# Kernel optimization log

Hardware: AMD Instinct MI355X
Metric: run time of the kernel (lower is better)

The kernel has to match this reference:

```python
import jax, jax.numpy as jnp
import numpy as np

B, N, D, U = 8, 2048, 512, 128


def setup_inputs() -> dict:
    key = jax.random.key(0)
    k_x, k_q, k_k, k_v, k_o = jax.random.split(key, 5)
    scale_in = 1.0 / np.sqrt(D)
    scale_u = 1.0 / np.sqrt(U)
    return {
        "inputs": jax.random.normal(k_x, (B, N, D), dtype=jnp.float32),
        "W_q": jax.random.normal(k_q, (D, U), dtype=jnp.float32) * scale_in,
        "W_k": jax.random.normal(k_k, (D, U), dtype=jnp.float32) * scale_in,
        "W_v": jax.random.normal(k_v, (D, U), dtype=jnp.float32) * scale_in,
        "W_o": jax.random.normal(k_o, (U, D), dtype=jnp.float32) * scale_u,
        "b_o": jnp.zeros((D,), dtype=jnp.float32),
    }


def reference(inputs, W_q, W_k, W_v, W_o, b_o):
    # Single-head scaled dot-product self-attention + output dense + residual
    Q = jnp.einsum('bnd,du->bnu', inputs, W_q)
    K = jnp.einsum('bnd,du->bnu', inputs, W_k)
    V = jnp.einsum('bnd,du->bnu', inputs, W_v)
    inv_sqrt_u = 1.0 / jnp.sqrt(jnp.asarray(W_q.shape[-1], inputs.dtype))
    scores = jnp.einsum('bnu,bmu->bnm', Q, K) * inv_sqrt_u  # [B,N,N]
    attn = jax.nn.softmax(scores, axis=-1)
    ctx = jnp.einsum('bnm,bmu->bnu', attn, V)  # [B,N,U]
    return jnp.einsum('bnu,ud->bnd', ctx, W_o) + b_o + inputs
```

## Files before the change

### kernel.cpp

```cpp
#include <hip/hip_runtime.h>

#define BB 8
#define NN 2048
#define DD 512
#define UU 128
#define SPLITS 4
#define KSPLIT 512

typedef __bf16 bf16_t;
typedef __bf16 bf16x4 __attribute__((ext_vector_type(4)));
typedef __bf16 bf16x8 __attribute__((ext_vector_type(8)));
typedef float floatx4 __attribute__((ext_vector_type(4)));

__device__ __forceinline__ floatx4 mfma16(bf16x8 a, bf16x8 b, floatx4 c) {
  return __builtin_amdgcn_mfma_f32_16x16x32_bf16(a, b, c, 0, 0, 0);
}

#define SW(r, g) ((((g) ^ ((r) & 7)) * 8))

__device__ __forceinline__ void gld_lds16(const bf16_t* g, bf16_t* l) {
  __builtin_amdgcn_global_load_lds(
      (const __attribute__((address_space(1))) unsigned int*)g,
      (__attribute__((address_space(3))) unsigned int*)l, 16, 0, 0);
}

__global__ __launch_bounds__(256) void cast_x_kernel(const float* __restrict__ x,
                                                     bf16_t* __restrict__ xb) {
  int G = blockIdx.x * 256 + threadIdx.x;
  int token = G >> 6;
  int g = G & 63;
  int dstg = (g & 56) | ((g & 7) ^ (token & 7));
  const float4* src = reinterpret_cast<const float4*>(x) + (size_t)G * 2;
  float4 a = src[0], b = src[1];
  bf16x8 o;
  o[0] = (bf16_t)a.x; o[1] = (bf16_t)a.y; o[2] = (bf16_t)a.z; o[3] = (bf16_t)a.w;
  o[4] = (bf16_t)b.x; o[5] = (bf16_t)b.y; o[6] = (bf16_t)b.z; o[7] = (bf16_t)b.w;
  *reinterpret_cast<bf16x8*>(&xb[(size_t)token * 512 + dstg * 8]) = o;
}

__global__ __launch_bounds__(256) void pack_w_kernel(const float* __restrict__ wq,
                                                     const float* __restrict__ wk,
                                                     const float* __restrict__ wv,
                                                     const float* __restrict__ wo,
                                                     bf16_t* __restrict__ wqkvt,
                                                     bf16_t* __restrict__ wot) {
  int gid = blockIdx.x * 256 + threadIdx.x;
  if (gid < 384 * 512) {
    int nrow = gid >> 9;
    int kdst = gid & 511;
    int ksrc = (kdst & ~56) | (((((kdst >> 3) & 7)) ^ (nrow & 7)) << 3);
    const float* src = (nrow < 128) ? wq : ((nrow < 256) ? wk : wv);
    int n = nrow & 127;
    wqkvt[gid] = (bf16_t)src[ksrc * 128 + n];
  } else {
    int g = gid - 384 * 512;
    int nrow = g >> 7;
    int kdst = g & 127;
    int ksrc = (kdst & ~56) | (((((kdst >> 3) & 7)) ^ (nrow & 7)) << 3);
    wot[g] = (bf16_t)wo[ksrc * 512 + nrow];
  }
}

__global__ __launch_bounds__(256, 4) void qkv_gemm_kernel(const bf16_t* __restrict__ xb,
                                                          const bf16_t* __restrict__ wqkvt,
                                                          bf16_t* __restrict__ Q,
                                                          bf16_t* __restrict__ K,
                                                          bf16_t* __restrict__ Vt) {
  __shared__ bf16_t lA[128 * 64];
  __shared__ bf16_t lB[64 * 64];
  const int lid = (blockIdx.x & 7) * 96 + (blockIdx.x >> 3);
  const int m0 = (lid / 6) * 128;
  const int n0 = (lid % 6) * 64;
  const int tid = threadIdx.x;
  const int w = tid >> 6, lane = tid & 63;
  const int quad = lane >> 4, l15 = lane & 15;

  floatx4 zero4 = {0.f, 0.f, 0.f, 0.f};
  floatx4 acc[2][4];
#pragma unroll
  for (int mi = 0; mi < 2; mi++)
#pragma unroll
    for (int nt = 0; nt < 4; nt++) acc[mi][nt] = zero4;

  for (int kc = 0; kc < 512; kc += 64) {
    __syncthreads();
#pragma unroll
    for (int i = 0; i < 4; i++) {
      int t = tid + i * 256;
      int r = t >> 3, g = t & 7;
      gld_lds16(&xb[(size_t)(m0 + r) * 512 + kc + g * 8], &lA[t * 8]);
    }
#pragma unroll
    for (int i = 0; i < 2; i++) {
      int t = tid + i * 256;
      int r = t >> 3, g = t & 7;
      gld_lds16(&wqkvt[(size_t)(n0 + r) * 512 + kc + g * 8], &lB[t * 8]);
    }
    asm volatile("s_waitcnt vmcnt(0)" ::: "memory");
    __syncthreads();
#pragma unroll
    for (int kb = 0; kb < 2; kb++) {
      bf16x8 bfr[4];
#pragma unroll
      for (int nt = 0; nt < 4; nt++)
        bfr[nt] = *reinterpret_cast<const bf16x8*>(
            &lB[(nt * 16 + l15) * 64 + SW(l15, kb * 4 + quad)]);
#pragma unroll
      for (int mi = 0; mi < 2; mi++) {
        bf16x8 a = *reinterpret_cast<const bf16x8*>(
            &lA[(w * 32 + mi * 16 + l15) * 64 + SW(l15, kb * 4 + quad)]);
#pragma unroll
        for (int nt = 0; nt < 4; nt++)
          acc[mi][nt] = mfma16(a, bfr[nt], acc[mi][nt]);
      }
    }
  }

#pragma unroll
  for (int mi = 0; mi < 2; mi++)
#pragma unroll
    for (int nt = 0; nt < 4; nt++) {
      int n = n0 + nt * 16 + l15;
#pragma unroll
      for (int r = 0; r < 4; r++) {
        int token = m0 + w * 32 + mi * 16 + quad * 4 + r;
        bf16_t h = (bf16_t)acc[mi][nt][r];
        if (n < 128) {
          Q[(size_t)token * 128 + n] = h;
        } else if (n < 256) {
          int nk = n - 128;
          int nsw = (nk & ~56) | ((((nk >> 3) & 7) ^ (token & 7)) << 3);
          K[(size_t)token * 128 + nsw] = h;
        } else {
          int bidx = token >> 11;
          int t = token & 2047;
          int u = n - 256;
          int tsw = (t & ~56) | ((((t >> 3) & 7) ^ (u & 7)) << 3);
          Vt[((size_t)bidx * 128 + u) * 2048 + tsw] = h;
        }
      }
    }
}

__global__ __launch_bounds__(256, 2) void attn_kernel(const bf16_t* __restrict__ Q,
                                                      const bf16_t* __restrict__ K,
                                                      const bf16_t* __restrict__ Vt,
                                                      bf16_t* __restrict__ Op,
                                                      float* __restrict__ ml) {
  __shared__ bf16_t lK[2][64 * 128];
  __shared__ bf16_t lV[2][128 * 64];
  __shared__ bf16_t lP[4][32 * 64];

  const int lid = (blockIdx.x & 7) * 64 + (blockIdx.x >> 3);
  const int qb = lid & 15;
  const int bs = lid >> 4;
  const int b = bs >> 2;
  const int s = bs & 3;
  const int tid = threadIdx.x;
  const int w = tid >> 6, lane = tid & 63;
  const int quad = lane >> 4, l15 = lane & 15;
  const float c = 0.08838834764831845f * 1.4426950408889634f;

  bf16x8 qf[2][4];
#pragma unroll
  for (int mt = 0; mt < 2; mt++) {
    const bf16_t* qrow =
        &Q[((size_t)b * NN + qb * 128 + w * 32 + mt * 16 + l15) * 128 + quad * 8];
#pragma unroll
    for (int kb = 0; kb < 4; kb++)
      qf[mt][kb] = *reinterpret_cast<const bf16x8*>(qrow + kb * 32);
  }

  float l_part[2] = {0.f, 0.f};
  floatx4 zero4 = {0.f, 0.f, 0.f, 0.f};
  floatx4 accO[2][8];
#pragma unroll
  for (int mt = 0; mt < 2; mt++)
#pragma unroll
    for (int ut = 0; ut < 8; ut++) accO[mt][ut] = zero4;

  bf16_t* pw = &lP[w][0];
  const int kt0 = s * KSPLIT;
  const bf16_t* kbase = &K[(size_t)b * NN * 128];
  const bf16_t* vbase = &Vt[(size_t)b * 128 * 2048];

  {
    const bf16_t* ksrc = kbase + (size_t)kt0 * 128;
#pragma unroll
    for (int i = 0; i < 4; i++) {
      int t = tid + i * 256;
      gld_lds16(ksrc + (size_t)t * 8, &lK[0][t * 8]);
    }
#pragma unroll
    for (int i = 0; i < 4; i++) {
      int t = tid + i * 256;
      int r = t >> 3, g = t & 7;
      gld_lds16(vbase + (size_t)r * 2048 + kt0 + g * 8, &lV[0][t * 8]);
    }
  }
  asm volatile("s_waitcnt vmcnt(0)" ::: "memory");
  __syncthreads();

  int cur = 0;
  for (int kt = kt0; kt < kt0 + KSPLIT; kt += 64) {
    if (kt + 64 < kt0 + KSPLIT) {
      const int nxt = kt + 64;
      const bf16_t* ksrc = kbase + (size_t)nxt * 128;
#pragma unroll
      for (int i = 0; i < 4; i++) {
        int t = tid + i * 256;
        gld_lds16(ksrc + (size_t)t * 8, &lK[cur ^ 1][t * 8]);
      }
#pragma unroll
      for (int i = 0; i < 4; i++) {
        int t = tid + i * 256;
        int r = t >> 3, g = t & 7;
        gld_lds16(vbase + (size_t)r * 2048 + nxt + g * 8, &lV[cur ^ 1][t * 8]);
      }
    }

    floatx4 accS[4][2];
#pragma unroll
    for (int km = 0; km < 4; km++)
#pragma unroll
      for (int mt = 0; mt < 2; mt++) accS[km][mt] = zero4;
    __builtin_amdgcn_s_setprio(1);
#pragma unroll
    for (int kb = 0; kb < 4; kb++) {
#pragma unroll
      for (int km = 0; km < 4; km++) {
        bf16x8 kf = *reinterpret_cast<const bf16x8*>(
            &lK[cur][(km * 16 + l15) * 128 + SW(l15, kb * 4 + quad)]);
#pragma unroll
        for (int mt = 0; mt < 2; mt++)
          accS[km][mt] = mfma16(kf, qf[mt][kb], accS[km][mt]);
      }
    }
    __builtin_amdgcn_s_setprio(0);

#pragma unroll
    for (int km = 0; km < 4; km++) {
#pragma unroll
      for (int mt = 0; mt < 2; mt++) {
        float p0 = __builtin_amdgcn_exp2f(accS[km][mt][0] * c);
        float p1 = __builtin_amdgcn_exp2f(accS[km][mt][1] * c);
        float p2 = __builtin_amdgcn_exp2f(accS[km][mt][2] * c);
        float p3 = __builtin_amdgcn_exp2f(accS[km][mt][3] * c);
        l_part[mt] += (p0 + p1) + (p2 + p3);
        bf16x4 pk;
        pk[0] = (bf16_t)p0; pk[1] = (bf16_t)p1; pk[2] = (bf16_t)p2; pk[3] = (bf16_t)p3;
        int row = mt * 16 + l15;
        int g = km * 2 + (quad >> 1);
        *reinterpret_cast<bf16x4*>(
            &pw[row * 64 + ((g ^ (row & 7)) * 8) + (quad & 1) * 4]) = pk;
      }
    }
    asm volatile("s_waitcnt lgkmcnt(0)" ::: "memory");

    __builtin_amdgcn_s_setprio(1);
#pragma unroll
    for (int kb = 0; kb < 2; kb++) {
      bf16x8 pa[2];
#pragma unroll
      for (int mt = 0; mt < 2; mt++)
        pa[mt] = *reinterpret_cast<const bf16x8*>(
            &pw[(mt * 16 + l15) * 64 + SW(l15, kb * 4 + quad)]);
#pragma unroll
      for (int ut = 0; ut < 8; ut++) {
        bf16x8 bv = *reinterpret_cast<const bf16x8*>(
            &lV[cur][(ut * 16 + l15) * 64 + SW(l15, kb * 4 + quad)]);
#pragma unroll
        for (int mt = 0; mt < 2; mt++)
          accO[mt][ut] = mfma16(pa[mt], bv, accO[mt][ut]);
      }
    }
    __builtin_amdgcn_s_setprio(0);

    asm volatile("s_waitcnt vmcnt(0)" ::: "memory");
    __syncthreads();
    cur ^= 1;
  }

#pragma unroll
  for (int mt = 0; mt < 2; mt++) {
    float v = l_part[mt];
    v += __shfl_xor(v, 16);
    v += __shfl_xor(v, 32);
    l_part[mt] = v;
  }

  size_t base = ((size_t)(b * 16 + qb) * SPLITS + s);
  bf16_t* op = Op + base * (128 * 128);
  float* mlp = ml + base * 128;
#pragma unroll
  for (int mt = 0; mt < 2; mt++)
#pragma unroll
    for (int ut = 0; ut < 8; ut++)
#pragma unroll
      for (int r = 0; r < 4; r++)
        op[(w * 32 + mt * 16 + quad * 4 + r) * 128 + ut * 16 + l15] =
            (bf16_t)accO[mt][ut][r];
  if (quad == 0) {
#pragma unroll
    for (int mt = 0; mt < 2; mt++) mlp[w * 32 + mt * 16 + l15] = l_part[mt];
  }
}

__global__ __launch_bounds__(256) void merge_kernel(const bf16_t* __restrict__ Op,
                                                    const float* __restrict__ ml,
                                                    bf16_t* __restrict__ ctx) {
  const int blk = blockIdx.x;
  const int qloc = blockIdx.y * 16 + (threadIdx.x >> 4);
  const int g = threadIdx.x & 15;

  float L = 0.f;
  float o[8];
#pragma unroll
  for (int j = 0; j < 8; j++) o[j] = 0.f;
#pragma unroll
  for (int s = 0; s < SPLITS; s++) {
    size_t e = (size_t)blk * SPLITS + s;
    L += ml[e * 128 + qloc];
    bf16x8 ch = *reinterpret_cast<const bf16x8*>(&Op[(e * 128 + qloc) * 128 + g * 8]);
#pragma unroll
    for (int j = 0; j < 8; j++) o[j] += (float)ch[j];
  }
  float inv = 1.0f / L;
  int gsw = (g & 8) | ((g & 7) ^ (qloc & 7));
  bf16x8 ch;
#pragma unroll
  for (int j = 0; j < 8; j++) ch[j] = (bf16_t)(o[j] * inv);
  const int bb = blk >> 4, qbl = blk & 15;
  *reinterpret_cast<bf16x8*>(
      &ctx[((size_t)bb * NN + qbl * 128 + qloc) * 128 + gsw * 8]) = ch;
}

__global__ __launch_bounds__(256, 4) void out_gemm_kernel(const bf16_t* __restrict__ ctx,
                                                          const bf16_t* __restrict__ wot,
                                                          const float* __restrict__ bo,
                                                          const float* __restrict__ x0,
                                                          float* __restrict__ out) {
  __shared__ bf16_t lA[64 * 128];
  __shared__ bf16_t lB[64 * 128];
  const int lid = (blockIdx.x & 7) * 256 + (blockIdx.x >> 3);
  const int m0 = (lid >> 3) * 64;
  const int n0 = (lid & 7) * 64;
  const int tid = threadIdx.x;
  const int w = tid >> 6, lane = tid & 63;
  const int quad = lane >> 4, l15 = lane & 15;

#pragma unroll
  for (int i = 0; i < 4; i++) {
    int t = tid + i * 256;
    gld_lds16(&ctx[(size_t)m0 * 128 + t * 8], &lA[t * 8]);
    gld_lds16(&wot[(size_t)n0 * 128 + t * 8], &lB[t * 8]);
  }
  asm volatile("s_waitcnt vmcnt(0)" ::: "memory");
  __syncthreads();

  floatx4 zero4 = {0.f, 0.f, 0.f, 0.f};
  floatx4 acc[4];
#pragma unroll
  for (int nt = 0; nt < 4; nt++) acc[nt] = zero4;
#pragma unroll
  for (int kb = 0; kb < 4; kb++) {
    bf16x8 a = *reinterpret_cast<const bf16x8*>(&lA[(w * 16 + l15) * 128 + SW(l15, kb * 4 + quad)]);
#pragma unroll
    for (int nt = 0; nt < 4; nt++) {
      bf16x8 bfr = *reinterpret_cast<const bf16x8*>(&lB[(nt * 16 + l15) * 128 + SW(l15, kb * 4 + quad)]);
      acc[nt] = mfma16(a, bfr, acc[nt]);
    }
  }

#pragma unroll
  for (int nt = 0; nt < 4; nt++) {
    int n = n0 + nt * 16 + l15;
    float bias = bo[n];
#pragma unroll
    for (int r = 0; r < 4; r++) {
      size_t m = m0 + w * 16 + quad * 4 + r;
      out[m * 512 + n] = acc[nt][r] + bias + x0[m * 512 + n];
    }
  }
}

extern "C" void kernel_launch(void* const* d_in, const int* in_sizes, int n_in,
                              void* d_out, int out_size, void* d_ws, size_t ws_size,
                              hipStream_t stream) {
  const float* x  = (const float*)d_in[0];
  const float* wq = (const float*)d_in[1];
  const float* wk = (const float*)d_in[2];
  const float* wv = (const float*)d_in[3];
  const float* wo = (const float*)d_in[4];
  const float* bo = (const float*)d_in[5];
  float* out = (float*)d_out;

  char* ws = (char*)d_ws;
  bf16_t* Qb    = (bf16_t*)(ws);
  bf16_t* Kb    = (bf16_t*)(ws + 4194304);
  bf16_t* Vt    = (bf16_t*)(ws + 2 * 4194304);
  bf16_t* Ctx   = (bf16_t*)(ws + 3 * 4194304);
  bf16_t* Wqkvt = (bf16_t*)(ws + 4 * 4194304);
  bf16_t* Wot   = (bf16_t*)(ws + 4 * 4194304 + 393216);
  bf16_t* Xb    = (bf16_t*)(ws + 4 * 4194304 + 524288);
  bf16_t* Op    = (bf16_t*)(ws + 4 * 4194304 + 524288);
  float*  ml    = (float*)(ws + 4 * 4194304 + 524288 + 33554432);

  cast_x_kernel<<<4096, 256, 0, stream>>>(x, Xb);
  pack_w_kernel<<<1024, 256, 0, stream>>>(wq, wk, wv, wo, Wqkvt, Wot);
  qkv_gemm_kernel<<<768, 256, 0, stream>>>(Xb, Wqkvt, Qb, Kb, Vt);
  attn_kernel<<<512, 256, 0, stream>>>(Qb, Kb, Vt, Op, ml);
  merge_kernel<<<dim3(128, 8), 256, 0, stream>>>(Op, ml, Ctx);
  out_gemm_kernel<<<2048, 256, 0, stream>>>(Ctx, Wot, bo, x, out);
}
```

Baseline: 148.2 us.

## Use 32x32x16 MFMA in attention and pass P through registers instead of LDS

The attention kernel moves from 16x16x32 bf16 MFMAs to 32x32x16 MFMAs for both QK^T and PV. The softmax probabilities are packed to bf16 and rearranged into the PV A-operand layout with cross-half-wave shuffles, so the per-wave LDS staging buffer for P and its wait are gone. This cuts LDS traffic and MFMA instruction count per tile, and the larger tile gives more reuse per fragment. The costs are extra shuffle and select instructions, a different register-pressure profile, and a new output write pattern.

New measurement: 146.8 us. About the same (-0.9%).

```diff
diff --git a/kernel.cpp b/kernel.cpp
--- a/kernel.cpp
+++ b/kernel.cpp
@@ -11,9 +11,19 @@
 typedef __bf16 bf16x4 __attribute__((ext_vector_type(4)));
 typedef __bf16 bf16x8 __attribute__((ext_vector_type(8)));
 typedef float floatx4 __attribute__((ext_vector_type(4)));
+typedef float floatx16 __attribute__((ext_vector_type(16)));
 
 __device__ __forceinline__ floatx4 mfma16(bf16x8 a, bf16x8 b, floatx4 c) {
   return __builtin_amdgcn_mfma_f32_16x16x32_bf16(a, b, c, 0, 0, 0);
+}
+__device__ __forceinline__ floatx16 mfma32(bf16x8 a, bf16x8 b, floatx16 c) {
+  return __builtin_amdgcn_mfma_f32_32x32x16_bf16(a, b, c, 0, 0, 0);
+}
+
+__device__ __forceinline__ unsigned int pk2(float a, float b) {
+  union { bf16_t x[2]; unsigned int u; } t;
+  t.x[0] = (bf16_t)a; t.x[1] = (bf16_t)b;
+  return t.u;
 }
 
 #define SW(r, g) ((((g) ^ ((r) & 7)) * 8))
@@ -149,7 +159,6 @@
                                                       float* __restrict__ ml) {
   __shared__ bf16_t lK[2][64 * 128];
   __shared__ bf16_t lV[2][128 * 64];
-  __shared__ bf16_t lP[4][32 * 64];
 
   const int lid = (blockIdx.x & 7) * 64 + (blockIdx.x >> 3);
   const int qb = lid & 15;
@@ -158,28 +167,25 @@
   const int s = bs & 3;
   const int tid = threadIdx.x;
   const int w = tid >> 6, lane = tid & 63;
-  const int quad = lane >> 4, l15 = lane & 15;
+  const int l31 = lane & 31, h = lane >> 5;
   const float c = 0.08838834764831845f * 1.4426950408889634f;
 
-  bf16x8 qf[2][4];
-#pragma unroll
-  for (int mt = 0; mt < 2; mt++) {
+  bf16x8 qf[8];
+  {
     const bf16_t* qrow =
-        &Q[((size_t)b * NN + qb * 128 + w * 32 + mt * 16 + l15) * 128 + quad * 8];
-#pragma unroll
-    for (int kb = 0; kb < 4; kb++)
-      qf[mt][kb] = *reinterpret_cast<const bf16x8*>(qrow + kb * 32);
-  }
-
-  float l_part[2] = {0.f, 0.f};
-  floatx4 zero4 = {0.f, 0.f, 0.f, 0.f};
-  floatx4 accO[2][8];
-#pragma unroll
-  for (int mt = 0; mt < 2; mt++)
-#pragma unroll
-    for (int ut = 0; ut < 8; ut++) accO[mt][ut] = zero4;
-
-  bf16_t* pw = &lP[w][0];
+        &Q[((size_t)b * NN + qb * 128 + w * 32 + l31) * 128 + h * 8];
+#pragma unroll
+    for (int kb = 0; kb < 8; kb++)
+      qf[kb] = *reinterpret_cast<const bf16x8*>(qrow + kb * 16);
+  }
+
+  float l_part = 0.f;
+  floatx16 accO[4];
+#pragma unroll
+  for (int ut = 0; ut < 4; ut++)
+#pragma unroll
+    for (int i = 0; i < 16; i++) accO[ut][i] = 0.f;
+
   const int kt0 = s * KSPLIT;
   const bf16_t* kbase = &K[(size_t)b * NN * 128];
   const bf16_t* vbase = &Vt[(size_t)b * 128 * 2048];
@@ -219,59 +225,62 @@
       }
     }
 
-    floatx4 accS[4][2];
-#pragma unroll
-    for (int km = 0; km < 4; km++)
-#pragma unroll
-      for (int mt = 0; mt < 2; mt++) accS[km][mt] = zero4;
+    floatx16 accS[2];
+#pragma unroll
+    for (int km = 0; km < 2; km++)
+#pragma unroll
+      for (int i = 0; i < 16; i++) accS[km][i] = 0.f;
+
     __builtin_amdgcn_s_setprio(1);
 #pragma unroll
-    for (int kb = 0; kb < 4; kb++) {
-#pragma unroll
-      for (int km = 0; km < 4; km++) {
+    for (int kb = 0; kb < 8; kb++) {
+#pragma unroll
+      for (int km = 0; km < 2; km++) {
+        int r = km * 32 + l31;
         bf16x8 kf = *reinterpret_cast<const bf16x8*>(
-            &lK[cur][(km * 16 + l15) * 128 + SW(l15, kb * 4 + quad)]);
-#pragma unroll
-        for (int mt = 0; mt < 2; mt++)
-          accS[km][mt] = mfma16(kf, qf[mt][kb], accS[km][mt]);
+            &lK[cur][r * 128 + SW(r, kb * 2 + h)]);
+        accS[km] = mfma32(kf, qf[kb], accS[km]);
       }
     }
     __builtin_amdgcn_s_setprio(0);
 
-#pragma unroll
-    for (int km = 0; km < 4; km++) {
-#pragma unroll
-      for (int mt = 0; mt < 2; mt++) {
-        float p0 = __builtin_amdgcn_exp2f(accS[km][mt][0] * c);
-        float p1 = __builtin_amdgcn_exp2f(accS[km][mt][1] * c);
-        float p2 = __builtin_amdgcn_exp2f(accS[km][mt][2] * c);
-        float p3 = __builtin_amdgcn_exp2f(accS[km][mt][3] * c);
-        l_part[mt] += (p0 + p1) + (p2 + p3);
-        bf16x4 pk;
-        pk[0] = (bf16_t)p0; pk[1] = (bf16_t)p1; pk[2] = (bf16_t)p2; pk[3] = (bf16_t)p3;
-        int row = mt * 16 + l15;
-        int g = km * 2 + (quad >> 1);
-        *reinterpret_cast<bf16x4*>(
-            &pw[row * 64 + ((g ^ (row & 7)) * 8) + (quad & 1) * 4]) = pk;
-      }
-    }
-    asm volatile("s_waitcnt lgkmcnt(0)" ::: "memory");
+    bf16x8 pa[4];
+#pragma unroll
+    for (int km = 0; km < 2; km++) {
+      float p[16];
+#pragma unroll
+      for (int i = 0; i < 16; i++) {
+        p[i] = __builtin_amdgcn_exp2f(accS[km][i] * c);
+        l_part += p[i];
+      }
+#pragma unroll
+      for (int s2 = 0; s2 < 2; s2++) {
+        unsigned int w00 = pk2(p[8 * s2 + 0], p[8 * s2 + 1]);
+        unsigned int w01 = pk2(p[8 * s2 + 2], p[8 * s2 + 3]);
+        unsigned int w10 = pk2(p[8 * s2 + 4], p[8 * s2 + 5]);
+        unsigned int w11 = pk2(p[8 * s2 + 6], p[8 * s2 + 7]);
+        unsigned int s0 = h ? w00 : w10;
+        unsigned int s1 = h ? w01 : w11;
+        unsigned int r0 = __shfl_xor(s0, 32);
+        unsigned int r1 = __shfl_xor(s1, 32);
+        union { unsigned int u[4]; bf16x8 v; } af;
+        af.u[0] = h ? r0 : w00;
+        af.u[1] = h ? r1 : w01;
+        af.u[2] = h ? w10 : r0;
+        af.u[3] = h ? w11 : r1;
+        pa[km * 2 + s2] = af.v;
+      }
+    }
 
     __builtin_amdgcn_s_setprio(1);
 #pragma unroll
-    for (int kb = 0; kb < 2; kb++) {
-      bf16x8 pa[2];
-#pragma unroll
-      for (int mt = 0; mt < 2; mt++)
-        pa[mt] = *reinterpret_cast<const bf16x8*>(
-            &pw[(mt * 16 + l15) * 64 + SW(l15, kb * 4 + quad)]);
-#pragma unroll
-      for (int ut = 0; ut < 8; ut++) {
-        bf16x8 bv = *reinterpret_cast<const bf16x8*>(
-            &lV[cur][(ut * 16 + l15) * 64 + SW(l15, kb * 4 + quad)]);
-#pragma unroll
-        for (int mt = 0; mt < 2; mt++)
-          accO[mt][ut] = mfma16(pa[mt], bv, accO[mt][ut]);
+    for (int ut = 0; ut < 4; ut++) {
+#pragma unroll
+      for (int ks = 0; ks < 4; ks++) {
+        int ur = ut * 32 + l31;
+        bf16x8 vf = *reinterpret_cast<const bf16x8*>(
+            &lV[cur][ur * 64 + SW(ur, ks * 2 + h)]);
+        accO[ut] = mfma32(pa[ks], vf, accO[ut]);
       }
     }
     __builtin_amdgcn_s_setprio(0);
@@ -281,29 +290,18 @@
     cur ^= 1;
   }
 
-#pragma unroll
-  for (int mt = 0; mt < 2; mt++) {
-    float v = l_part[mt];
-    v += __shfl_xor(v, 16);
-    v += __shfl_xor(v, 32);
-    l_part[mt] = v;
-  }
+  l_part += __shfl_xor(l_part, 32);
 
   size_t base = ((size_t)(b * 16 + qb) * SPLITS + s);
   bf16_t* op = Op + base * (128 * 128);
-  float* mlp = ml + base * 128;
-#pragma unroll
-  for (int mt = 0; mt < 2; mt++)
-#pragma unroll
-    for (int ut = 0; ut < 8; ut++)
-#pragma unroll
-      for (int r = 0; r < 4; r++)
-        op[(w * 32 + mt * 16 + quad * 4 + r) * 128 + ut * 16 + l15] =
-            (bf16_t)accO[mt][ut][r];
-  if (quad == 0) {
-#pragma unroll
-    for (int mt = 0; mt < 2; mt++) mlp[w * 32 + mt * 16 + l15] = l_part[mt];
-  }
+#pragma unroll
+  for (int ut = 0; ut < 4; ut++)
+#pragma unroll
+    for (int i = 0; i < 16; i++) {
+      int qr = w * 32 + (i & 3) + 8 * (i >> 2) + 4 * h;
+      op[qr * 128 + ut * 32 + l31] = (bf16_t)accO[ut][i];
+    }
+  if (h == 0) ml[base * 128 + w * 32 + l31] = l_part;
 }
 
 __global__ __launch_bounds__(256) void merge_kernel(const bf16_t* __restrict__ Op,
```
